# Kernel tuning notes

Hardware: AMD Instinct MI355X
Metric: run time of the kernel (lower is better)

Reference implementation:

```python
import jax, jax.numpy as jnp
import numpy as np

# Real spherical harmonics, l=2 (2l+1 = 5 components), standard normalization.
C_XY   = float(0.5  * np.sqrt(15.0 / np.pi))
C_Z2   = float(0.25 * np.sqrt(5.0  / np.pi))
C_X2Y2 = float(0.25 * np.sqrt(15.0 / np.pi))

N_NODES  = 50000
N_EDGES  = 1_600_000
HIDDEN   = 32
CHANNELS = 16


def _sph_harm_l2(u):
    # u: [E,3] unit vectors -> [E,5]
    x, y, z = u[..., 0], u[..., 1], u[..., 2]
    return jnp.stack([
        C_XY * x * y,
        C_XY * y * z,
        C_Z2 * (3.0 * z * z - 1.0),
        C_XY * x * z,
        C_X2Y2 * (x * x - y * y),
    ], axis=-1)


def setup_inputs() -> dict:
    key = jax.random.key(0)
    k = jax.random.split(key, 6)
    positions = jax.random.normal(k[0], (N_NODES, 3), dtype=jnp.float32) * 10.0
    edge_index = jax.random.randint(k[1], (2, N_EDGES), 0, N_NODES)
    # radial MLP: dist [E,1] -> relu -> [E,CHANNELS]
    W1 = jax.random.normal(k[2], (1, HIDDEN), dtype=jnp.float32)
    b1 = jax.random.normal(k[3], (HIDDEN,), dtype=jnp.float32) * 0.1
    W2 = jax.random.normal(k[4], (HIDDEN, CHANNELS), dtype=jnp.float32) / np.sqrt(HIDDEN)
    b2 = jax.random.normal(k[5], (CHANNELS,), dtype=jnp.float32) * 0.1
    return {"positions": positions, "W1": W1, "b1": b1, "W2": W2, "b2": b2,
            "edge_index": edge_index}


def reference(positions, W1, b1, W2, b2, edge_index):
    i_arr = edge_index[0]
    j_arr = edge_index[1]
    # per-edge relative vectors + distances (point_cloud.getVectors / getDistance)
    rel = positions[i_arr] - positions[j_arr]            # [E,3]
    dist = jnp.linalg.norm(rel, axis=-1, keepdims=True)  # [E,1]
    dist = jnp.maximum(dist, 1e-8)                       # guard degenerate edges
    unit = rel / dist                                    # normalized vectors
    sh = _sph_harm_l2(unit)                              # [E,5] spharm(l_filter)
    # calculateRadialValues: radial MLP on distances -> [E,CHANNELS]
    h = jax.nn.relu(dist @ W1 + b1)
    radial = h @ W2 + b2
    # filter = spherical harmonics broadcast * per-channel radial values
    return radial[:, :, None] * sh[:, None, :]           # [E,CHANNELS,5]
```

## Files before the change

### kernel.cpp

```cpp
#include <hip/hip_runtime.h>
#include <math.h>

#define E_CNT 1600000
#define HID 32
#define CH 16
#define NSEG 33
#define TABF (2 * CH * NSEG)
#define TILE 256
#define GRID (E_CNT / TILE)
#define ESTR 9

#define C_XY   1.0925484305920792f
#define C_Z2   0.31539156525252005f
#define C_X2Y2 0.5462742152960396f

typedef float f32x4 __attribute__((ext_vector_type(4)));

__global__ void precompute_kernel(const float* __restrict__ W1,
                                  const float* __restrict__ b1,
                                  const float* __restrict__ W2,
                                  const float* __restrict__ b2,
                                  float* __restrict__ ws) {
    __shared__ float s_v[HID], s_w1[HID], s_b1[HID];
    __shared__ int s_rank[HID];
    int tid = threadIdx.x;
    if (tid < HID) {
        float w = W1[tid], b = b1[tid];
        float v = 0.0f;
        if (w != 0.0f) v = fmaxf(-b / w, 0.0f);
        s_v[tid] = v; s_w1[tid] = w; s_b1[tid] = b;
    }
    __syncthreads();
    if (tid < HID) {
        float v = s_v[tid];
        int r = 0;
        for (int k = 0; k < HID; ++k) {
            float vk = s_v[k];
            r += (vk < v || (vk == v && k < tid)) ? 1 : 0;
        }
        s_rank[tid] = r;
        ws[tid] = v;
    }
    __syncthreads();
    if (tid < NSEG * CH) {
        int m = tid / CH;
        int c = tid % CH;
        float A = 0.0f, B = b2[c];
        for (int k = 0; k < HID; ++k) {
            float w = s_w1[k], b = s_b1[k];
            bool act;
            if (w > 0.0f)      act = (s_rank[k] < m);
            else if (w < 0.0f) act = (s_rank[k] >= m);
            else               act = (b > 0.0f);
            if (act) {
                float w2 = W2[k * CH + c];
                A = fmaf(w, w2, A);
                B = fmaf(b, w2, B);
            }
        }
        ws[32 + c * NSEG + m]             = A;
        ws[32 + CH * NSEG + c * NSEG + m] = B;
    }
}

__global__ __launch_bounds__(TILE, 8) void edge_kernel(const float* __restrict__ pos,
                                                       const int* __restrict__ ei,
                                                       const float* __restrict__ ws,
                                                       float* __restrict__ out) {
    __shared__ float sTab[TABF];
    __shared__ float sE[TILE * ESTR];

    const int t = threadIdx.x;
    const int e = blockIdx.x * TILE + t;

    const int ni = ei[e];
    const int nj = ei[E_CNT + e];

    for (int q = t; q < TABF; q += TILE) sTab[q] = ws[32 + q];

    float vbp[HID];
#pragma unroll
    for (int k = 0; k < HID; ++k) vbp[k] = ws[k];

    const float* pi = pos + 3 * ni;
    const float* pj = pos + 3 * nj;
    const float rx = pi[0] - pj[0];
    const float ry = pi[1] - pj[1];
    const float rz = pi[2] - pj[2];

    const float d2   = fmaf(rx, rx, fmaf(ry, ry, rz * rz));
    const float dist = fmaxf(sqrtf(d2), 1e-8f);
    const float inv  = __builtin_amdgcn_rcpf(dist);
    const float x = rx * inv, y = ry * inv, z = rz * inv;

    float* row_w = &sE[t * ESTR];
    row_w[0] = C_XY * x * y;
    row_w[1] = C_XY * y * z;
    row_w[2] = C_Z2 * fmaf(3.0f * z, z, -1.0f);
    row_w[3] = C_XY * x * z;
    row_w[4] = C_X2Y2 * (x * x - y * y);
    row_w[5] = dist;

    int m = 0;
#pragma unroll
    for (int k = 0; k < HID; ++k) m += (vbp[k] < dist) ? 1 : 0;
    row_w[6] = __int_as_float(m);

    __syncthreads();

    f32x4* ob = reinterpret_cast<f32x4*>(out) + (size_t)blockIdx.x * (TILE * 20) + t;
#pragma unroll
    for (int it = 0; it < 20; ++it) {
        const int idx4 = t + TILE * it;
        const int el = idx4 / 20;
        const int u  = idx4 - el * 20;
        const int p  = 4 * u;
        const int rA  =  p      / 5;
        const int ri1 = (p + 1) / 5;
        const int ri2 = (p + 2) / 5;
        const int rB  = (p + 3) / 5;
        const int si0 =  p      - 5 * rA;
        const int si1 = (p + 1) - 5 * ri1;
        const int si2 = (p + 2) - 5 * ri2;
        const int si3 = (p + 3) - 5 * rB;
        const float* row = &sE[el * ESTR];
        const float d = row[5];
        const int   mm = __float_as_int(row[6]);
        const float rvA = fmaf(d, sTab[rA * NSEG + mm], sTab[CH * NSEG + rA * NSEG + mm]);
        const float rvB = fmaf(d, sTab[rB * NSEG + mm], sTab[CH * NSEG + rB * NSEG + mm]);
        f32x4 o;
        o.x = rvA * row[si0];
        o.y = (ri1 == rA ? rvA : rvB) * row[si1];
        o.z = (ri2 == rA ? rvA : rvB) * row[si2];
        o.w = rvB * row[si3];
        __builtin_nontemporal_store(o, ob + it * TILE);
    }
}

extern "C" void kernel_launch(void* const* d_in, const int* in_sizes, int n_in,
                              void* d_out, int out_size, void* d_ws, size_t ws_size,
                              hipStream_t stream) {
    const float* pos = (const float*)d_in[0];
    const float* W1  = (const float*)d_in[1];
    const float* b1  = (const float*)d_in[2];
    const float* W2  = (const float*)d_in[3];
    const float* b2  = (const float*)d_in[4];
    const int*   ei  = (const int*)d_in[5];
    float* out = (float*)d_out;
    float* ws  = (float*)d_ws;

    precompute_kernel<<<1, 544, 0, stream>>>(W1, b1, W2, b2, ws);
    edge_kernel<<<GRID, TILE, 0, stream>>>(pos, ei, ws, out);
}
```

Baseline: 113.3 us.

## Use persistent grid-stride blocks with edge-index prefetch and per-wave LDS staging

```diff
diff --git a/kernel.cpp b/kernel.cpp
--- a/kernel.cpp
+++ b/kernel.cpp
@@ -7,7 +7,8 @@
 #define NSEG 33
 #define TABF (2 * CH * NSEG)
 #define TILE 256
-#define GRID (E_CNT / TILE)
+#define NTILES (E_CNT / TILE)
+#define GRIDP 2048
 #define ESTR 9
 
 #define C_XY   1.0925484305920792f
@@ -71,10 +72,8 @@
     __shared__ float sE[TILE * ESTR];
 
     const int t = threadIdx.x;
-    const int e = blockIdx.x * TILE + t;
-
-    const int ni = ei[e];
-    const int nj = ei[E_CNT + e];
+    const int w = t >> 6;
+    const int l = t & 63;
 
     for (int q = t; q < TABF; q += TILE) sTab[q] = ws[32 + q];
 
@@ -82,58 +81,69 @@
 #pragma unroll
     for (int k = 0; k < HID; ++k) vbp[k] = ws[k];
 
-    const float* pi = pos + 3 * ni;
-    const float* pj = pos + 3 * nj;
-    const float rx = pi[0] - pj[0];
-    const float ry = pi[1] - pj[1];
-    const float rz = pi[2] - pj[2];
-
-    const float d2   = fmaf(rx, rx, fmaf(ry, ry, rz * rz));
-    const float dist = fmaxf(sqrtf(d2), 1e-8f);
-    const float inv  = __builtin_amdgcn_rcpf(dist);
-    const float x = rx * inv, y = ry * inv, z = rz * inv;
-
-    float* row_w = &sE[t * ESTR];
-    row_w[0] = C_XY * x * y;
-    row_w[1] = C_XY * y * z;
-    row_w[2] = C_Z2 * fmaf(3.0f * z, z, -1.0f);
-    row_w[3] = C_XY * x * z;
-    row_w[4] = C_X2Y2 * (x * x - y * y);
-    row_w[5] = dist;
-
-    int m = 0;
-#pragma unroll
-    for (int k = 0; k < HID; ++k) m += (vbp[k] < dist) ? 1 : 0;
-    row_w[6] = __int_as_float(m);
+    int T = blockIdx.x;
+    int cNi = ei[T * TILE + t];
+    int cNj = ei[E_CNT + T * TILE + t];
 
     __syncthreads();
 
-    f32x4* ob = reinterpret_cast<f32x4*>(out) + (size_t)blockIdx.x * (TILE * 20) + t;
+    float* row_w = &sE[t * ESTR];
+    const float* rowbase = &sE[(w * 64) * ESTR];
+
+    for (; T < NTILES; T += GRIDP) {
+        int nNi = 0, nNj = 0;
+        const int Tn = T + GRIDP;
+        if (Tn < NTILES) {
+            nNi = ei[Tn * TILE + t];
+            nNj = ei[E_CNT + Tn * TILE + t];
+        }
+
+        const float* pi = pos + 3 * cNi;
+        const float* pj = pos + 3 * cNj;
+        const float rx = pi[0] - pj[0];
+        const float ry = pi[1] - pj[1];
+        const float rz = pi[2] - pj[2];
+        const float d2   = fmaf(rx, rx, fmaf(ry, ry, rz * rz));
+        const float dist = fmaxf(sqrtf(d2), 1e-8f);
+        const float inv  = __builtin_amdgcn_rcpf(dist);
+        const float x = rx * inv, y = ry * inv, z = rz * inv;
+        row_w[0] = C_XY * x * y;
+        row_w[1] = C_XY * y * z;
+        row_w[2] = C_Z2 * fmaf(3.0f * z, z, -1.0f);
+        row_w[3] = C_XY * x * z;
+        row_w[4] = C_X2Y2 * (x * x - y * y);
+        row_w[5] = dist;
+        int m = 0;
 #pragma unroll
-    for (int it = 0; it < 20; ++it) {
-        const int idx4 = t + TILE * it;
-        const int el = idx4 / 20;
-        const int u  = idx4 - el * 20;
-        const int p  = 4 * u;
-        const int rA  =  p      / 5;
-        const int ri1 = (p + 1) / 5;
-        const int ri2 = (p + 2) / 5;
-        const int rB  = (p + 3) / 5;
-        const int si0 =  p      - 5 * rA;
-        const int si1 = (p + 1) - 5 * ri1;
-        const int si2 = (p + 2) - 5 * ri2;
-        const int si3 = (p + 3) - 5 * rB;
-        const float* row = &sE[el * ESTR];
-        const float d = row[5];
-        const int   mm = __float_as_int(row[6]);
-        const float rvA = fmaf(d, sTab[rA * NSEG + mm], sTab[CH * NSEG + rA * NSEG + mm]);
-        const float rvB = fmaf(d, sTab[rB * NSEG + mm], sTab[CH * NSEG + rB * NSEG + mm]);
-        f32x4 o;
-        o.x = rvA * row[si0];
-        o.y = (ri1 == rA ? rvA : rvB) * row[si1];
-        o.z = (ri2 == rA ? rvA : rvB) * row[si2];
-        o.w = rvB * row[si3];
-        __builtin_nontemporal_store(o, ob + it * TILE);
+        for (int k = 0; k < HID; ++k) m += (vbp[k] < dist) ? 1 : 0;
+        row_w[6] = __int_as_float(m);
+
+        f32x4* ob = reinterpret_cast<f32x4*>(out)
+                  + ((size_t)T * TILE + w * 64) * 20 + l;
+#pragma unroll
+        for (int it = 0; it < 20; ++it) {
+            const int idx4 = l + 64 * it;
+            const int el = idx4 / 20;
+            const int u  = idx4 - el * 20;
+            const int p  = 4 * u;
+            const int rA  =  p      / 5, si0 =  p      - 5 * rA;
+            const int ri1 = (p + 1) / 5, si1 = (p + 1) - 5 * ri1;
+            const int ri2 = (p + 2) / 5, si2 = (p + 2) - 5 * ri2;
+            const int rB  = (p + 3) / 5, si3 = (p + 3) - 5 * rB;
+            const float* row = rowbase + el * ESTR;
+            const float d = row[5];
+            const int   mm = __float_as_int(row[6]);
+            const float rvA = fmaf(d, sTab[rA * NSEG + mm], sTab[CH * NSEG + rA * NSEG + mm]);
+            const float rvB = fmaf(d, sTab[rB * NSEG + mm], sTab[CH * NSEG + rB * NSEG + mm]);
+            f32x4 o;
+            o.x = rvA * row[si0];
+            o.y = (ri1 == rA ? rvA : rvB) * row[si1];
+            o.z = (ri2 == rA ? rvA : rvB) * row[si2];
+            o.w = rvB * row[si3];
+            __builtin_nontemporal_store(o, ob + it * 64);
+        }
+
+        cNi = nNi; cNj = nNj;
     }
 }
 
@@ -150,5 +160,5 @@
     float* ws  = (float*)d_ws;
 
     precompute_kernel<<<1, 544, 0, stream>>>(W1, b1, W2, b2, ws);
-    edge_kernel<<<GRID, TILE, 0, stream>>>(pos, ei, ws, out);
+    edge_kernel<<<GRIDP, TILE, 0, stream>>>(pos, ei, ws, out);
 }
```

New measurement: 218.7 us. 1.93x slower.
